# Kernel tuning notes

Measured on AMD Instinct MI355X. Metric: run time of the kernel, lower is better.

Reference implementation:

```python
import math
import jax, jax.numpy as jnp
import numpy as np

B, N, E, R = 1024, 200, 256, 256

def _layernorm(x, g, b, eps=1e-5):
    mu = x.mean(-1, keepdims=True)
    var = ((x - mu) ** 2).mean(-1, keepdims=True)
    return (x - mu) / jnp.sqrt(var + eps) * g + b

def setup_inputs() -> dict:
    key = jax.random.key(0)
    ks = jax.random.split(key, 16)
    d = {}
    d["e_emb"] = jax.random.normal(ks[0], (B, E), jnp.float32)
    d["nb_rel"] = jax.random.normal(ks[1], (B, N, R), jnp.float32)
    d["delta_t"] = jax.random.uniform(ks[2], (B, N), jnp.float32) * 10.0
    d["r_emb"] = jax.random.normal(ks[3], (B, R), jnp.float32)
    d["hist_mask"] = jax.random.randint(ks[4], (B, N), 0, 2).astype(bool)
    d["rel_w"] = jax.random.normal(ks[5], (E, R), jnp.float32) / math.sqrt(R)
    d["log_tau1"] = jnp.asarray(1.0, jnp.float32)
    d["log_tau2"] = jnp.asarray(2.5, jnp.float32)
    d["sharpness"] = jnp.asarray(1.5, jnp.float32)
    d["log_gamma"] = jnp.asarray(-2.0, jnp.float32)
    d["attn_w"] = jax.random.normal(ks[6], (3, E, E), jnp.float32) / math.sqrt(E)
    d["sp_w"] = jax.random.normal(ks[7], (3, E, 6 * E), jnp.float32) / math.sqrt(6 * E)
    d["sp_b"] = jnp.zeros((3, E), jnp.float32)
    d["ln_g"] = jnp.ones((3, E), jnp.float32)
    d["ln_b"] = jnp.zeros((3, E), jnp.float32)
    d["csq_w"] = jax.random.normal(ks[8], (E, R), jnp.float32) / math.sqrt(R)
    d["csq_b"] = jnp.zeros((E,), jnp.float32)
    d["csl_w"] = jax.random.normal(ks[9], (3, E), jnp.float32) / math.sqrt(E)
    d["csl_b"] = jnp.zeros((3,), jnp.float32)
    d["on_g"] = jnp.ones((E,), jnp.float32)
    d["on_b"] = jnp.zeros((E,), jnp.float32)
    return d

def _pna_one_scale(msgs, mask, e_emb, q_key, attn_w, sp_w, sp_b, ln_g, ln_b):
    # msgs: [B,N,E], mask: [B,N] bool, e_emb: [B,E], q_key: [B,E]
    valid_f = mask[..., None].astype(msgs.dtype)
    n_valid = jnp.maximum(mask.astype(msgs.dtype).sum(1, keepdims=True), 1.0)  # [B,1]
    msgs_v = msgs * valid_f
    mean_v = msgs_v.sum(1) / n_valid
    max_v = msgs_v.max(1)
    min_v = jnp.clip(jnp.where(mask[..., None], msgs, 10000.0).min(1), -10000.0, 10000.0)
    sq_m = (jnp.clip(msgs_v, -10.0, 10.0) ** 2).sum(1) / n_valid
    std_v = jnp.sqrt(jnp.maximum(sq_m - mean_v ** 2, 1e-6))
    q_proj = q_key @ attn_w.T  # [B,E]
    attn_raw = jnp.einsum('bne,be->bn', msgs, q_proj) / math.sqrt(msgs.shape[-1])
    attn_raw = jnp.where(mask, attn_raw, -10000.0)
    all_invalid = ~mask.any(1, keepdims=True)  # [B,1]
    attn_raw = jnp.where(all_invalid, 0.0, attn_raw)
    attn_p = jax.nn.softmax(attn_raw, axis=-1)
    attn_v = jnp.einsum('bn,bne->be', attn_p, msgs)
    feats = jnp.concatenate([mean_v, max_v, min_v, std_v, attn_v, e_emb], axis=-1)  # [B,6E]
    h = feats @ sp_w.T + sp_b
    h = _layernorm(h, ln_g, ln_b)
    return jax.nn.gelu(h, approximate=False)  # dropout = identity (eval mode)

def reference(e_emb, nb_rel, delta_t, r_emb, hist_mask, rel_w, log_tau1, log_tau2,
              sharpness, log_gamma, attn_w, sp_w, sp_b, ln_g, ln_b,
              csq_w, csq_b, csl_w, csl_b, on_g, on_b):
    msgs = jnp.einsum('bnr,er->bne', nb_rel, rel_w)
    gamma = jnp.exp(log_gamma)
    decay = jnp.exp(-gamma * jnp.maximum(delta_t, 0.0))
    msgs_dec = msgs * decay[..., None]
    tau1 = jnp.exp(log_tau1)
    tau2 = jnp.exp(log_tau2) + tau1
    sharp = jnp.clip(sharpness, 0.1, 5.0)
    w_fine = jax.nn.sigmoid(-sharp * (delta_t - tau1))
    w_coarse = jax.nn.sigmoid(sharp * (delta_t - tau2))
    w_mid = jnp.maximum(1.0 - w_fine - w_coarse, 0.0)
    scale_w = jnp.stack([w_fine, w_mid, w_coarse])  # [3,B,N]
    m_scales = msgs_dec[None] * scale_w[..., None]  # [3,B,N,E]
    q_key = r_emb @ rel_w.T  # [B,E]
    pna_v = jax.vmap(_pna_one_scale, in_axes=(0, None, None, None, 0, 0, 0, 0, 0))
    scales = pna_v(m_scales, hist_mask, e_emb, q_key, attn_w, sp_w, sp_b, ln_g, ln_b)  # [3,B,E]
    sq = r_emb @ csq_w.T + csq_b  # [B,E]
    logits = sq @ csl_w.T + csl_b  # [B,3]
    weights = jax.nn.softmax(logits, axis=-1)
    out = jnp.einsum('bs,sbe->be', weights, scales)
    return _layernorm(out, on_g, on_b)  # drop = identity (eval)
```

## Files before the change

### kernel.cpp

```cpp
#include <hip/hip_runtime.h>
#include <hip/hip_bf16.h>
#include <math.h>

#define B_   1024
#define N_   200
#define NR_  208
#define NT_  13
#define E_   256
#define R_   256
#define K6_  1536

typedef __attribute__((ext_vector_type(8))) short bf16x8;
typedef __attribute__((ext_vector_type(4))) float f32x4;

__device__ __forceinline__ unsigned short f2bf(float f) {
  unsigned int u = __float_as_uint(f);
  u += 0x7fffu + ((u >> 16) & 1u);
  return (unsigned short)(u >> 16);
}

__device__ __forceinline__ unsigned int pk_bf(float lo, float hi) {
  float2 t; t.x = lo; t.y = hi;
  __hip_bfloat162 h = __float22bfloat162_rn(t);
  unsigned int u;
  __builtin_memcpy(&u, &h, 4);
  return u;
}

__device__ __forceinline__ float gelu_exact(float x) {
  return 0.5f * x * (1.f + erff(x * 0.70710678118654752f));
}

__global__ __launch_bounds__(256) void k_cast(
    const float* __restrict__ rel_w, const float* __restrict__ sp_w,
    const float* __restrict__ csq_w, const float* __restrict__ attn_w,
    unsigned short* __restrict__ rwf, unsigned short* __restrict__ spwf,
    float* __restrict__ rwT, float* __restrict__ cwT, float* __restrict__ awT) {
  int o = blockIdx.x * 256 + threadIdx.x;
  if (o < 65536) {
    int j = o & 7, r16 = (o >> 3) & 15, quad = (o >> 7) & 3, ks = (o >> 9) & 7, et = o >> 12;
    rwf[o] = f2bf(rel_w[(size_t)(et * 16 + r16) * 256 + ks * 32 + quad * 8 + j]);
    return;
  }
  o -= 65536;
  if (o < 1179648) {
    int j = o & 7, r16 = (o >> 3) & 15, quad = (o >> 7) & 3, ks = (o >> 9) & 7;
    int rest = o >> 12;
    int kc = rest % 6, se = rest / 6;
    int et = se & 15, s = se >> 4;
    spwf[o] = f2bf(sp_w[(size_t)(s * 256 + et * 16 + r16) * 1536 + kc * 256 + ks * 32 + quad * 8 + j]);
    return;
  }
  o -= 1179648;
  if (o < 65536) { int r = o >> 8, e = o & 255; rwT[o] = rel_w[(size_t)e * 256 + r]; return; }
  o -= 65536;
  if (o < 65536) { int r = o >> 8, e = o & 255; cwT[o] = csq_w[(size_t)e * 256 + r]; return; }
  o -= 65536;
  if (o < 196608) {
    int s = o >> 16, rem = o & 65535, ep = rem >> 8, e = rem & 255;
    awT[o] = attn_w[((size_t)s * 256 + e) * 256 + ep];
  }
}

__global__ __launch_bounds__(256) void k_prep(
    const float* __restrict__ r_emb, const float* __restrict__ rwT,
    const float* __restrict__ cwT, const float* __restrict__ awT,
    const float* __restrict__ csq_b, const float* __restrict__ csl_w,
    const float* __restrict__ csl_b, const float* __restrict__ rel_w,
    unsigned short* __restrict__ t_bf, float* __restrict__ wts) {
  __shared__ __align__(16) float re[4][256];
  __shared__ __align__(16) float qk[4][256];
  __shared__ __align__(16) float sqs[4][256];
  __shared__ __align__(16) float qp[3][4][256];
  __shared__ float lg[4][3];
  int b0 = blockIdx.x * 4;
  int tid = threadIdx.x;
  int e = tid;
#pragma unroll
  for (int i = 0; i < 4; ++i)
    re[i][tid] = r_emb[(size_t)(b0 + i) * 256 + tid];
  __syncthreads();
  {
    float qkv[4], sv[4];
#pragma unroll
    for (int i = 0; i < 4; ++i) { qkv[i] = 0.f; sv[i] = 0.f; }
    for (int g = 0; g < 64; ++g) {
      float4 xi[4];
#pragma unroll
      for (int i = 0; i < 4; ++i) xi[i] = ((const float4*)re[i])[g];
#pragma unroll
      for (int k = 0; k < 4; ++k) {
        int r = g * 4 + k;
        float w = rwT[(size_t)r * 256 + e];
        float c = cwT[(size_t)r * 256 + e];
#pragma unroll
        for (int i = 0; i < 4; ++i) {
          float x = (k == 0) ? xi[i].x : (k == 1) ? xi[i].y : (k == 2) ? xi[i].z : xi[i].w;
          qkv[i] = fmaf(w, x, qkv[i]);
          sv[i]  = fmaf(c, x, sv[i]);
        }
      }
    }
    float cb = csq_b[e];
#pragma unroll
    for (int i = 0; i < 4; ++i) {
      qk[i][e] = qkv[i];
      sqs[i][e] = sv[i] + cb;
    }
  }
  __syncthreads();
  if (tid < 12) {
    int i = tid / 3, k = tid % 3;
    float acc = csl_b[k];
    for (int ee = 0; ee < 256; ++ee) acc += sqs[i][ee] * csl_w[k * 256 + ee];
    lg[i][k] = acc;
  }
  __syncthreads();
  if (tid < 4) {
    float l0 = lg[tid][0], l1 = lg[tid][1], l2 = lg[tid][2];
    float m = fmaxf(l0, fmaxf(l1, l2));
    float e0 = expf(l0 - m), e1 = expf(l1 - m), e2 = expf(l2 - m);
    float inv = 1.f / (e0 + e1 + e2);
    wts[(b0 + tid) * 4 + 0] = e0 * inv;
    wts[(b0 + tid) * 4 + 1] = e1 * inv;
    wts[(b0 + tid) * 4 + 2] = e2 * inv;
  }
  {
    float qpv[3][4];
#pragma unroll
    for (int s = 0; s < 3; ++s)
#pragma unroll
      for (int i = 0; i < 4; ++i) qpv[s][i] = 0.f;
    for (int g = 0; g < 64; ++g) {
      float4 qf[4];
#pragma unroll
      for (int i = 0; i < 4; ++i) qf[i] = ((const float4*)qk[i])[g];
#pragma unroll
      for (int k = 0; k < 4; ++k) {
        int ep = g * 4 + k;
#pragma unroll
        for (int s = 0; s < 3; ++s) {
          float w = awT[((size_t)s * 256 + ep) * 256 + e];
#pragma unroll
          for (int i = 0; i < 4; ++i) {
            float x = (k == 0) ? qf[i].x : (k == 1) ? qf[i].y : (k == 2) ? qf[i].z : qf[i].w;
            qpv[s][i] = fmaf(w, x, qpv[s][i]);
          }
        }
      }
    }
    __syncthreads();
#pragma unroll
    for (int s = 0; s < 3; ++s)
#pragma unroll
      for (int i = 0; i < 4; ++i) qp[s][i][e] = qpv[s][i];
  }
  __syncthreads();
  {
    int r = tid;
    float tacc[3][4];
#pragma unroll
    for (int s = 0; s < 3; ++s)
#pragma unroll
      for (int i = 0; i < 4; ++i) tacc[s][i] = 0.f;
    for (int e4 = 0; e4 < 64; ++e4) {
      float4 qv[3][4];
#pragma unroll
      for (int s = 0; s < 3; ++s)
#pragma unroll
        for (int i = 0; i < 4; ++i)
          qv[s][i] = ((const float4*)qp[s][i])[e4];
#pragma unroll
      for (int j = 0; j < 4; ++j) {
        float w = rel_w[(size_t)(e4 * 4 + j) * 256 + r];
#pragma unroll
        for (int s = 0; s < 3; ++s)
#pragma unroll
          for (int i = 0; i < 4; ++i) {
            float q = (j == 0) ? qv[s][i].x : (j == 1) ? qv[s][i].y
                      : (j == 2) ? qv[s][i].z : qv[s][i].w;
            tacc[s][i] = fmaf(q, w, tacc[s][i]);
          }
      }
    }
#pragma unroll
    for (int s = 0; s < 3; ++s)
#pragma unroll
      for (int i = 0; i < 4; ++i)
        t_bf[((size_t)(b0 + i) * 3 + s) * 256 + r] = f2bf(tacc[s][i]);
  }
}

__global__ __launch_bounds__(1024, 4) void k1_main(
    const float* __restrict__ nb_rel, const float* __restrict__ delta_t,
    const unsigned char* __restrict__ hm_raw, const float* __restrict__ e_emb,
    const float* __restrict__ p_lt1, const float* __restrict__ p_lt2,
    const float* __restrict__ p_sh, const float* __restrict__ p_lgm,
    const unsigned short* __restrict__ rwf, const unsigned short* __restrict__ t_bf,
    unsigned short* __restrict__ feats) {
  __shared__ __align__(16) struct {
    unsigned int a[NR_ * 132];
    float c[3][NR_];
    float p[3][NR_];
    float nmeta[NR_ * 12];
  } sm;
  int b = blockIdx.x;
  int tid = threadIdx.x;
  int lane = tid & 63, wave = tid >> 6;
  int row16 = lane & 15, quad = lane >> 4;

  int hasNZoff = 0, hasFP = 0;
  {
    unsigned char cc = hm_raw[tid];
    if ((tid & 3) != 0 && cc != 0) {
      hasNZoff = 1;
      if (cc == 0x3Fu || cc == 0x80u) hasFP = 1;
    }
  }
  int cntNZ = __syncthreads_count(hasNZoff);
  int cntFP = __syncthreads_count(hasFP);
  int mmode = (cntNZ == 0) ? 0 : (cntFP > 0 ? 2 : 1);

  float tau1 = __expf(p_lt1[0]);
  float tau2 = __expf(p_lt2[0]) + tau1;
  float sharp = fminf(fmaxf(p_sh[0], 0.1f), 5.0f);
  float gamma = __expf(p_lgm[0]);

  bool mk = false;
  if (tid < NR_) {
    float mf = 0.f, c0 = 0.f, c1 = 0.f, c2 = 0.f;
    if (tid < N_) {
      size_t mi = (size_t)b * N_ + tid;
      if (mmode == 0)      mk = ((const int*)hm_raw)[mi] != 0;
      else if (mmode == 1) mk = hm_raw[mi] != 0;
      else                 mk = ((const float*)hm_raw)[mi] != 0.f;
      float dt = delta_t[mi];
      mf = mk ? 1.f : 0.f;
      float decay = __expf(-gamma * fmaxf(dt, 0.f));
      float wf = 1.f / (1.f + __expf(sharp * (dt - tau1)));
      float wc = 1.f / (1.f + __expf(-sharp * (dt - tau2)));
      float wm = fmaxf(1.f - wf - wc, 0.f);
      c0 = decay * wf; c1 = decay * wm; c2 = decay * wc;
    }
    sm.c[0][tid] = c0; sm.c[1][tid] = c1; sm.c[2][tid] = c2;
    f32x4 w0, w1;
    w0[0] = mf * c0; w0[1] = mf * c1; w0[2] = mf * c2; w0[3] = mk ? 0.f : 1e4f;
    w1[0] = 0.f; w1[1] = 0.f; w1[2] = 0.f; w1[3] = mf;
    *(f32x4*)&sm.nmeta[tid * 12]     = w0;
    *(f32x4*)&sm.nmeta[tid * 12 + 4] = w1;
  }
  int cnt = __syncthreads_count(mk ? 1 : 0);
  float nvf = fmaxf((float)cnt, 1.f);
  bool allinv = (cnt == 0);

  {
    const float* src = nb_rel + (size_t)b * N_ * 256;
    float4 xs[NT_];
#pragma unroll
    for (int i = 0; i < NT_; ++i) {
      int n = i * 16 + wave;
      int gn = (n < N_) ? n : (N_ - 1);
      xs[i] = *(const float4*)(src + (size_t)gn * 256 + lane * 4);
    }
#pragma unroll
    for (int i = 0; i < NT_; ++i) {
      uint2 pk;
      pk.x = pk_bf(xs[i].x, xs[i].y);
      pk.y = pk_bf(xs[i].z, xs[i].w);
      *(uint2*)&sm.a[(i * 16 + wave) * 132 + lane * 2] = pk;
    }
  }
  __syncthreads();

  if (wave < NT_) {
    bf16x8 tfrag[8];
    {
      int sr = (row16 < 3) ? row16 : 0;
      const unsigned short* tb = t_bf + ((size_t)b * 3 + sr) * 256 + quad * 8;
      bf16x8 zer = {0, 0, 0, 0, 0, 0, 0, 0};
#pragma unroll
      for (int ks = 0; ks < 8; ++ks) {
        bf16x8 tv = *(const bf16x8*)(tb + ks * 32);
        tfrag[ks] = (row16 < 3) ? tv : zer;
      }
    }
    f32x4 acc;
#pragma unroll
    for (int cc = 0; cc < 4; ++cc) acc[cc] = 0.f;
#pragma unroll
    for (int ks = 0; ks < 8; ++ks) {
      bf16x8 af = *(const bf16x8*)&sm.a[(wave * 16 + row16) * 132 + ks * 16 + quad * 4];
      acc = __builtin_amdgcn_mfma_f32_16x16x32_bf16(af, tfrag[ks], acc, 0, 0, 0);
    }
    if (row16 < 3) {
#pragma unroll
      for (int rg = 0; rg < 4; ++rg) {
        int n = wave * 16 + quad * 4 + rg;
        float cw = sm.c[row16][n];
        float mf = sm.nmeta[n * 12 + 7];
        float l = cw * acc[rg] * 0.0625f;
        l = (mf > 0.5f) ? l : -1e4f;
        if (allinv) l = (n < N_) ? 0.f : -1e4f;
        sm.p[row16][n] = l;
      }
    }
  } else if (wave == NT_) {
    for (int i = lane; i < 256; i += 64) {
      unsigned short v = f2bf(e_emb[(size_t)b * 256 + i]);
      feats[((size_t)0 * B_ + b) * K6_ + 1280 + i] = v;
      feats[((size_t)1 * B_ + b) * K6_ + 1280 + i] = v;
      feats[((size_t)2 * B_ + b) * K6_ + 1280 + i] = v;
    }
  }

  bf16x8 bfr[8];
  {
#pragma unroll
    for (int ks = 0; ks < 8; ++ks)
      bfr[ks] = *(const bf16x8*)(rwf + ((((size_t)wave * 8 + ks) * 4 + quad) * 16 + row16) * 8);
  }
  __syncthreads();

  if (wave < 3) {
    int s = wave;
    float m = -1e30f;
    for (int n = lane; n < NR_; n += 64) m = fmaxf(m, sm.p[s][n]);
#pragma unroll
    for (int o = 32; o >= 1; o >>= 1) m = fmaxf(m, __shfl_xor(m, o, 64));
    float ssum = 0.f;
    for (int n = lane; n < NR_; n += 64) {
      float ev = __expf(sm.p[s][n] - m);
      sm.p[s][n] = ev;
      ssum += ev;
    }
#pragma unroll
    for (int o = 32; o >= 1; o >>= 1) ssum += __shfl_xor(ssum, o, 64);
    float inv = 1.f / ssum;
    for (int n = lane; n < NR_; n += 64)
      sm.nmeta[n * 12 + 4 + s] = sm.p[s][n] * inv * sm.c[s][n];
  }
  __syncthreads();

  float s_mean[3], s_mx[3], s_mn[3], s_sq[3], s_av[3];
#pragma unroll
  for (int s = 0; s < 3; ++s) {
    s_mean[s] = 0.f; s_mx[s] = -1e30f; s_mn[s] = 1e30f;
    s_sq[s] = 0.f; s_av[s] = 0.f;
  }

  for (int nt = 0; nt < NT_; ++nt) {
    f32x4 acc;
#pragma unroll
    for (int cc = 0; cc < 4; ++cc) acc[cc] = 0.f;
#pragma unroll
    for (int ks = 0; ks < 8; ++ks) {
      bf16x8 af = *(const bf16x8*)&sm.a[(nt * 16 + row16) * 132 + ks * 16 + quad * 4];
      acc = __builtin_amdgcn_mfma_f32_16x16x32_bf16(af, bfr[ks], acc, 0, 0, 0);
    }
    int nb = nt * 16 + quad * 4;
#pragma unroll
    for (int rg = 0; rg < 4; ++rg) {
      const float* nm = &sm.nmeta[(size_t)(nb + rg) * 12];
      f32x4 w0 = *(const f32x4*)nm;
      f32x4 w1 = *(const f32x4*)(nm + 4);
      float m = acc[rg];
#pragma unroll
      for (int s = 0; s < 3; ++s) {
        float vm = w0[s] * m;
        s_mean[s] += vm;
        s_mx[s] = fmaxf(s_mx[s], vm);
        s_mn[s] = fminf(s_mn[s], fmaf(w0[s], m, w0[3]));
        float cv = fminf(fmaxf(vm, -10.f), 10.f);
        s_sq[s] = fmaf(cv, cv, s_sq[s]);
        s_av[s] = fmaf(w1[s], m, s_av[s]);
      }
    }
  }

#pragma unroll
  for (int s = 0; s < 3; ++s) {
    float vmean = s_mean[s];
    vmean += __shfl_xor(vmean, 16, 64); vmean += __shfl_xor(vmean, 32, 64);
    float vmx = s_mx[s];
    vmx = fmaxf(vmx, __shfl_xor(vmx, 16, 64)); vmx = fmaxf(vmx, __shfl_xor(vmx, 32, 64));
    float vmn = s_mn[s];
    vmn = fminf(vmn, __shfl_xor(vmn, 16, 64)); vmn = fminf(vmn, __shfl_xor(vmn, 32, 64));
    float vsq = s_sq[s];
    vsq += __shfl_xor(vsq, 16, 64); vsq += __shfl_xor(vsq, 32, 64);
    float vav = s_av[s];
    vav += __shfl_xor(vav, 16, 64); vav += __shfl_xor(vav, 32, 64);
    if (lane < 16) {
      int e = wave * 16 + lane;
      size_t base = ((size_t)s * B_ + b) * K6_;
      float meanv = vmean / nvf;
      float stdv = sqrtf(fmaxf(vsq / nvf - meanv * meanv, 1e-6f));
      float mnv = fminf(fmaxf(vmn, -1e4f), 1e4f);
      feats[base + e] = f2bf(meanv);
      feats[base + 256 + e] = f2bf(vmx);
      feats[base + 512 + e] = f2bf(mnv);
      feats[base + 768 + e] = f2bf(stdv);
      feats[base + 1024 + e] = f2bf(vav);
    }
  }
}

__global__ __launch_bounds__(256) void k2_kernel(
    const unsigned short* __restrict__ feats, const unsigned short* __restrict__ spwf,
    const float* __restrict__ sp_b, float* __restrict__ hbuf) {
  __shared__ __align__(16) unsigned short A[16][1544];
  int id = blockIdx.x;
  int s = id >> 8;
  int rem = id & 255;
  int b0 = (rem >> 2) * 16;
  int e0 = (rem & 3) * 64;
  int tid = threadIdx.x, lane = tid & 63, wave = tid >> 6;
  int row16 = lane & 15, quad = lane >> 4;

  bf16x8 v[12];
#pragma unroll
  for (int t = 0; t < 12; ++t) {
    int j = tid + t * 256;
    int rw = j / 192, ck = j % 192;
    v[t] = *(const bf16x8*)(feats + ((size_t)s * B_ + b0 + rw) * K6_ + ck * 8);
  }
#pragma unroll
  for (int t = 0; t < 12; ++t) {
    int j = tid + t * 256;
    int rw = j / 192, ck = j % 192;
    *(bf16x8*)&A[rw][ck * 8] = v[t];
  }
  __syncthreads();

  int et = (e0 >> 4) + wave;
  const unsigned short* bp = spwf + (((size_t)s * 16 + et) * 6) * 4096;
  f32x4 acc;
#pragma unroll
  for (int cc = 0; cc < 4; ++cc) acc[cc] = 0.f;
#pragma unroll
  for (int kc = 0; kc < 6; ++kc) {
#pragma unroll
    for (int ks = 0; ks < 8; ++ks) {
      bf16x8 af = *(const bf16x8*)&A[row16][kc * 256 + ks * 32 + quad * 8];
      bf16x8 bf = *(const bf16x8*)(bp + ((size_t)(kc * 8 + ks) * 4 + quad) * 128 + row16 * 8);
      acc = __builtin_amdgcn_mfma_f32_16x16x32_bf16(af, bf, acc, 0, 0, 0);
    }
  }
  {
    int e = e0 + wave * 16 + row16;
    float bias = sp_b[s * 256 + e];
#pragma unroll
    for (int rg = 0; rg < 4; ++rg) {
      int rw = quad * 4 + rg;
      hbuf[((size_t)s * B_ + b0 + rw) * 256 + e] = acc[rg] + bias;
    }
  }
}

__global__ __launch_bounds__(256) void k3_kernel(
    const float* __restrict__ hbuf, const float* __restrict__ wts,
    const float* __restrict__ ln_g, const float* __restrict__ ln_b,
    const float* __restrict__ on_g, const float* __restrict__ on_b,
    float* __restrict__ out) {
  __shared__ float rs[4], rq[4];
  int b = blockIdx.x, tid = threadIdx.x, lane = tid & 63, wave = tid >> 6;
  float o = 0.f;
#pragma unroll
  for (int s = 0; s < 3; ++s) {
    float h = hbuf[((size_t)s * B_ + b) * 256 + tid];
    float sum = h, sq = h * h;
#pragma unroll
    for (int off = 32; off >= 1; off >>= 1) {
      sum += __shfl_xor(sum, off, 64);
      sq += __shfl_xor(sq, off, 64);
    }
    if (lane == 0) { rs[wave] = sum; rq[wave] = sq; }
    __syncthreads();
    float ts = rs[0] + rs[1] + rs[2] + rs[3];
    float tq = rq[0] + rq[1] + rq[2] + rq[3];
    __syncthreads();
    float mu = ts * (1.f / 256.f);
    float var = tq * (1.f / 256.f) - mu * mu;
    float rstd = rsqrtf(var + 1e-5f);
    float v = (h - mu) * rstd * ln_g[s * 256 + tid] + ln_b[s * 256 + tid];
    o += wts[b * 4 + s] * gelu_exact(v);
  }
  float sum = o, sq = o * o;
#pragma unroll
  for (int off = 32; off >= 1; off >>= 1) {
    sum += __shfl_xor(sum, off, 64);
    sq += __shfl_xor(sq, off, 64);
  }
  if (lane == 0) { rs[wave] = sum; rq[wave] = sq; }
  __syncthreads();
  float ts = rs[0] + rs[1] + rs[2] + rs[3];
  float tq = rq[0] + rq[1] + rq[2] + rq[3];
  float mu = ts * (1.f / 256.f);
  float var = tq * (1.f / 256.f) - mu * mu;
  float rstd = rsqrtf(var + 1e-5f);
  out[(size_t)b * 256 + tid] = (o - mu) * rstd * on_g[tid] + on_b[tid];
}

extern "C" void kernel_launch(void* const* d_in, const int* in_sizes, int n_in,
                              void* d_out, int out_size, void* d_ws, size_t ws_size,
                              hipStream_t stream) {
  const float* e_emb   = (const float*)d_in[0];
  const float* nb_rel  = (const float*)d_in[1];
  const float* delta_t = (const float*)d_in[2];
  const float* r_emb   = (const float*)d_in[3];
  const unsigned char* hist_mask = (const unsigned char*)d_in[4];
  const float* rel_w   = (const float*)d_in[5];
  const float* lt1     = (const float*)d_in[6];
  const float* lt2     = (const float*)d_in[7];
  const float* shp     = (const float*)d_in[8];
  const float* lgm     = (const float*)d_in[9];
  const float* attn_w  = (const float*)d_in[10];
  const float* sp_w    = (const float*)d_in[11];
  const float* sp_b    = (const float*)d_in[12];
  const float* ln_g    = (const float*)d_in[13];
  const float* ln_b    = (const float*)d_in[14];
  const float* csq_w   = (const float*)d_in[15];
  const float* csq_b   = (const float*)d_in[16];
  const float* csl_w   = (const float*)d_in[17];
  const float* csl_b   = (const float*)d_in[18];
  const float* on_g    = (const float*)d_in[19];
  const float* on_b    = (const float*)d_in[20];
  float* out = (float*)d_out;

  char* ws = (char*)d_ws;
  unsigned short* rwf   = (unsigned short*)(ws + 0);
  unsigned short* spwf  = (unsigned short*)(ws + 131072);
  unsigned short* t_bf  = (unsigned short*)(ws + 2490368);
  float* wts    = (float*)(ws + 4063232);
  unsigned short* feats = (unsigned short*)(ws + 4079616);
  float* hbuf   = (float*)(ws + 13516800);
  float* rwT    = (float*)(ws + 16662528);
  float* cwT    = (float*)(ws + 16924672);
  float* awT    = (float*)(ws + 17186816);

  hipLaunchKernelGGL(k_cast, dim3(6144), dim3(256), 0, stream, rel_w, sp_w, csq_w, attn_w,
                     rwf, spwf, rwT, cwT, awT);
  hipLaunchKernelGGL(k_prep, dim3(256), dim3(256), 0, stream, r_emb, rwT, cwT, awT,
                     csq_b, csl_w, csl_b, rel_w, t_bf, wts);
  hipLaunchKernelGGL(k1_main, dim3(1024), dim3(1024), 0, stream, nb_rel, delta_t, hist_mask,
                     e_emb, lt1, lt2, shp, lgm, rwf, t_bf, feats);
  hipLaunchKernelGGL(k2_kernel, dim3(768), dim3(256), 0, stream, feats, spwf, sp_b, hbuf);
  hipLaunchKernelGGL(k3_kernel, dim3(1024), dim3(256), 0, stream, hbuf, wts, ln_g, ln_b,
                     on_g, on_b, out);
}
```

Before: 484.2 us.

## Split prep kernel into three stages with two rows per block

The single prep kernel, which handled 4 batch rows per block in 256 blocks, becomes three kernels (q_key/sq plus softmax weights, attention projection, rel_w back-projection). Each handles 2 rows per block over 512 blocks, with intermediates staged in the feats and hbuf workspace buffers. The logits reduction now uses wave shuffles instead of 12 serial threads. The aim is more blocks across CUs and shorter dependent chains, at the cost of two extra launches, more global round trips, and weights reread by twice as many blocks.

```diff
diff --git a/kernel.cpp b/kernel.cpp
--- a/kernel.cpp
+++ b/kernel.cpp
@@ -62,133 +62,142 @@
   }
 }
 
-__global__ __launch_bounds__(256) void k_prep(
+__global__ __launch_bounds__(256) void k_prep1(
     const float* __restrict__ r_emb, const float* __restrict__ rwT,
-    const float* __restrict__ cwT, const float* __restrict__ awT,
-    const float* __restrict__ csq_b, const float* __restrict__ csl_w,
-    const float* __restrict__ csl_b, const float* __restrict__ rel_w,
-    unsigned short* __restrict__ t_bf, float* __restrict__ wts) {
-  __shared__ __align__(16) float re[4][256];
-  __shared__ __align__(16) float qk[4][256];
-  __shared__ __align__(16) float sqs[4][256];
-  __shared__ __align__(16) float qp[3][4][256];
-  __shared__ float lg[4][3];
-  int b0 = blockIdx.x * 4;
+    const float* __restrict__ cwT, const float* __restrict__ csq_b,
+    const float* __restrict__ csl_w, const float* __restrict__ csl_b,
+    float* __restrict__ qk_ws, float* __restrict__ wts) {
+  __shared__ __align__(16) float re[2][256];
+  __shared__ float sqs[2][256];
+  __shared__ float red[2][3][4];
+  int b0 = blockIdx.x * 2;
+  int tid = threadIdx.x, lane = tid & 63, wave = tid >> 6;
+  int e = tid;
+#pragma unroll
+  for (int i = 0; i < 2; ++i)
+    re[i][tid] = r_emb[(size_t)(b0 + i) * 256 + tid];
+  __syncthreads();
+  float qkv[2] = {0.f, 0.f}, sv[2] = {0.f, 0.f};
+  for (int g = 0; g < 64; ++g) {
+    float4 x0 = ((const float4*)re[0])[g];
+    float4 x1 = ((const float4*)re[1])[g];
+#pragma unroll
+    for (int k = 0; k < 4; ++k) {
+      int r = g * 4 + k;
+      float w = rwT[(size_t)r * 256 + e];
+      float c = cwT[(size_t)r * 256 + e];
+      float xa = (k == 0) ? x0.x : (k == 1) ? x0.y : (k == 2) ? x0.z : x0.w;
+      float xb = (k == 0) ? x1.x : (k == 1) ? x1.y : (k == 2) ? x1.z : x1.w;
+      qkv[0] = fmaf(w, xa, qkv[0]); qkv[1] = fmaf(w, xb, qkv[1]);
+      sv[0]  = fmaf(c, xa, sv[0]);  sv[1]  = fmaf(c, xb, sv[1]);
+    }
+  }
+  float cb = csq_b[e];
+#pragma unroll
+  for (int i = 0; i < 2; ++i) {
+    qk_ws[(size_t)(b0 + i) * 256 + e] = qkv[i];
+    sqs[i][e] = sv[i] + cb;
+  }
+  __syncthreads();
+#pragma unroll
+  for (int i = 0; i < 2; ++i)
+#pragma unroll
+    for (int k = 0; k < 3; ++k) {
+      float v = sqs[i][tid] * csl_w[k * 256 + tid];
+#pragma unroll
+      for (int o = 32; o >= 1; o >>= 1) v += __shfl_xor(v, o, 64);
+      if (lane == 0) red[i][k][wave] = v;
+    }
+  __syncthreads();
+  if (tid < 2) {
+    int i = tid;
+    float l[3];
+#pragma unroll
+    for (int k = 0; k < 3; ++k)
+      l[k] = csl_b[k] + red[i][k][0] + red[i][k][1] + red[i][k][2] + red[i][k][3];
+    float m = fmaxf(l[0], fmaxf(l[1], l[2]));
+    float e0 = expf(l[0] - m), e1 = expf(l[1] - m), e2 = expf(l[2] - m);
+    float inv = 1.f / (e0 + e1 + e2);
+    wts[(b0 + i) * 4 + 0] = e0 * inv;
+    wts[(b0 + i) * 4 + 1] = e1 * inv;
+    wts[(b0 + i) * 4 + 2] = e2 * inv;
+  }
+}
+
+__global__ __launch_bounds__(256) void k_prep2(
+    const float* __restrict__ qk_ws, const float* __restrict__ awT,
+    float* __restrict__ qp_ws) {
+  __shared__ __align__(16) float qk[2][256];
+  int b0 = blockIdx.x * 2;
   int tid = threadIdx.x;
   int e = tid;
 #pragma unroll
-  for (int i = 0; i < 4; ++i)
-    re[i][tid] = r_emb[(size_t)(b0 + i) * 256 + tid];
-  __syncthreads();
-  {
-    float qkv[4], sv[4];
-#pragma unroll
-    for (int i = 0; i < 4; ++i) { qkv[i] = 0.f; sv[i] = 0.f; }
-    for (int g = 0; g < 64; ++g) {
-      float4 xi[4];
-#pragma unroll
-      for (int i = 0; i < 4; ++i) xi[i] = ((const float4*)re[i])[g];
-#pragma unroll
-      for (int k = 0; k < 4; ++k) {
-        int r = g * 4 + k;
-        float w = rwT[(size_t)r * 256 + e];
-        float c = cwT[(size_t)r * 256 + e];
-#pragma unroll
-        for (int i = 0; i < 4; ++i) {
-          float x = (k == 0) ? xi[i].x : (k == 1) ? xi[i].y : (k == 2) ? xi[i].z : xi[i].w;
-          qkv[i] = fmaf(w, x, qkv[i]);
-          sv[i]  = fmaf(c, x, sv[i]);
-        }
+  for (int i = 0; i < 2; ++i)
+    qk[i][tid] = qk_ws[(size_t)(b0 + i) * 256 + tid];
+  __syncthreads();
+  float qpv[3][2];
+#pragma unroll
+  for (int s = 0; s < 3; ++s) { qpv[s][0] = 0.f; qpv[s][1] = 0.f; }
+  for (int g = 0; g < 64; ++g) {
+    float4 q0 = ((const float4*)qk[0])[g];
+    float4 q1 = ((const float4*)qk[1])[g];
+#pragma unroll
+    for (int k = 0; k < 4; ++k) {
+      int ep = g * 4 + k;
+      float xa = (k == 0) ? q0.x : (k == 1) ? q0.y : (k == 2) ? q0.z : q0.w;
+      float xb = (k == 0) ? q1.x : (k == 1) ? q1.y : (k == 2) ? q1.z : q1.w;
+#pragma unroll
+      for (int s = 0; s < 3; ++s) {
+        float w = awT[((size_t)s * 256 + ep) * 256 + e];
+        qpv[s][0] = fmaf(w, xa, qpv[s][0]);
+        qpv[s][1] = fmaf(w, xb, qpv[s][1]);
       }
     }
-    float cb = csq_b[e];
-#pragma unroll
-    for (int i = 0; i < 4; ++i) {
-      qk[i][e] = qkv[i];
-      sqs[i][e] = sv[i] + cb;
-    }
-  }
-  __syncthreads();
-  if (tid < 12) {
-    int i = tid / 3, k = tid % 3;
-    float acc = csl_b[k];
-    for (int ee = 0; ee < 256; ++ee) acc += sqs[i][ee] * csl_w[k * 256 + ee];
-    lg[i][k] = acc;
-  }
-  __syncthreads();
-  if (tid < 4) {
-    float l0 = lg[tid][0], l1 = lg[tid][1], l2 = lg[tid][2];
-    float m = fmaxf(l0, fmaxf(l1, l2));
-    float e0 = expf(l0 - m), e1 = expf(l1 - m), e2 = expf(l2 - m);
-    float inv = 1.f / (e0 + e1 + e2);
-    wts[(b0 + tid) * 4 + 0] = e0 * inv;
-    wts[(b0 + tid) * 4 + 1] = e1 * inv;
-    wts[(b0 + tid) * 4 + 2] = e2 * inv;
-  }
-  {
-    float qpv[3][4];
+  }
+#pragma unroll
+  for (int i = 0; i < 2; ++i)
 #pragma unroll
     for (int s = 0; s < 3; ++s)
-#pragma unroll
-      for (int i = 0; i < 4; ++i) qpv[s][i] = 0.f;
-    for (int g = 0; g < 64; ++g) {
-      float4 qf[4];
-#pragma unroll
-      for (int i = 0; i < 4; ++i) qf[i] = ((const float4*)qk[i])[g];
-#pragma unroll
-      for (int k = 0; k < 4; ++k) {
-        int ep = g * 4 + k;
-#pragma unroll
-        for (int s = 0; s < 3; ++s) {
-          float w = awT[((size_t)s * 256 + ep) * 256 + e];
-#pragma unroll
-          for (int i = 0; i < 4; ++i) {
-            float x = (k == 0) ? qf[i].x : (k == 1) ? qf[i].y : (k == 2) ? qf[i].z : qf[i].w;
-            qpv[s][i] = fmaf(w, x, qpv[s][i]);
-          }
-        }
+      qp_ws[((size_t)(b0 + i) * 3 + s) * 256 + e] = qpv[s][i];
+}
+
+__global__ __launch_bounds__(256) void k_prep3(
+    const float* __restrict__ qp_ws, const float* __restrict__ rel_w,
+    unsigned short* __restrict__ t_bf) {
+  __shared__ __align__(16) float qp[2][3][256];
+  int b0 = blockIdx.x * 2;
+  int tid = threadIdx.x;
+  int r = tid;
+  for (int j = tid; j < 2 * 3 * 256; j += 256)
+    ((float*)qp)[j] = qp_ws[(size_t)b0 * 768 + j];
+  __syncthreads();
+  float tacc[3][2];
+#pragma unroll
+  for (int s = 0; s < 3; ++s) { tacc[s][0] = 0.f; tacc[s][1] = 0.f; }
+  for (int e4 = 0; e4 < 64; ++e4) {
+    float4 qv[3][2];
+#pragma unroll
+    for (int s = 0; s < 3; ++s) {
+      qv[s][0] = ((const float4*)qp[0][s])[e4];
+      qv[s][1] = ((const float4*)qp[1][s])[e4];
+    }
+#pragma unroll
+    for (int j = 0; j < 4; ++j) {
+      float w = rel_w[(size_t)(e4 * 4 + j) * 256 + r];
+#pragma unroll
+      for (int s = 0; s < 3; ++s) {
+        float qa = (j == 0) ? qv[s][0].x : (j == 1) ? qv[s][0].y : (j == 2) ? qv[s][0].z : qv[s][0].w;
+        float qb = (j == 0) ? qv[s][1].x : (j == 1) ? qv[s][1].y : (j == 2) ? qv[s][1].z : qv[s][1].w;
+        tacc[s][0] = fmaf(qa, w, tacc[s][0]);
+        tacc[s][1] = fmaf(qb, w, tacc[s][1]);
       }
     }
-    __syncthreads();
+  }
+#pragma unroll
+  for (int i = 0; i < 2; ++i)
 #pragma unroll
     for (int s = 0; s < 3; ++s)
-#pragma unroll
-      for (int i = 0; i < 4; ++i) qp[s][i][e] = qpv[s][i];
-  }
-  __syncthreads();
-  {
-    int r = tid;
-    float tacc[3][4];
-#pragma unroll
-    for (int s = 0; s < 3; ++s)
-#pragma unroll
-      for (int i = 0; i < 4; ++i) tacc[s][i] = 0.f;
-    for (int e4 = 0; e4 < 64; ++e4) {
-      float4 qv[3][4];
-#pragma unroll
-      for (int s = 0; s < 3; ++s)
-#pragma unroll
-        for (int i = 0; i < 4; ++i)
-          qv[s][i] = ((const float4*)qp[s][i])[e4];
-#pragma unroll
-      for (int j = 0; j < 4; ++j) {
-        float w = rel_w[(size_t)(e4 * 4 + j) * 256 + r];
-#pragma unroll
-        for (int s = 0; s < 3; ++s)
-#pragma unroll
-          for (int i = 0; i < 4; ++i) {
-            float q = (j == 0) ? qv[s][i].x : (j == 1) ? qv[s][i].y
-                      : (j == 2) ? qv[s][i].z : qv[s][i].w;
-            tacc[s][i] = fmaf(q, w, tacc[s][i]);
-          }
-      }
-    }
-#pragma unroll
-    for (int s = 0; s < 3; ++s)
-#pragma unroll
-      for (int i = 0; i < 4; ++i)
-        t_bf[((size_t)(b0 + i) * 3 + s) * 256 + r] = f2bf(tacc[s][i]);
-  }
+      t_bf[((size_t)(b0 + i) * 3 + s) * 256 + r] = f2bf(tacc[s][i]);
 }
 
 __global__ __launch_bounds__(1024, 4) void k1_main(
@@ -537,10 +546,15 @@
   float* cwT    = (float*)(ws + 16924672);
   float* awT    = (float*)(ws + 17186816);
 
+  float* qk_ws = (float*)feats;
+  float* qp_ws = hbuf;
+
   hipLaunchKernelGGL(k_cast, dim3(6144), dim3(256), 0, stream, rel_w, sp_w, csq_w, attn_w,
                      rwf, spwf, rwT, cwT, awT);
-  hipLaunchKernelGGL(k_prep, dim3(256), dim3(256), 0, stream, r_emb, rwT, cwT, awT,
-                     csq_b, csl_w, csl_b, rel_w, t_bf, wts);
+  hipLaunchKernelGGL(k_prep1, dim3(512), dim3(256), 0, stream, r_emb, rwT, cwT,
+                     csq_b, csl_w, csl_b, qk_ws, wts);
+  hipLaunchKernelGGL(k_prep2, dim3(512), dim3(256), 0, stream, qk_ws, awT, qp_ws);
+  hipLaunchKernelGGL(k_prep3, dim3(512), dim3(256), 0, stream, qp_ws, rel_w, t_bf);
   hipLaunchKernelGGL(k1_main, dim3(1024), dim3(1024), 0, stream, nb_rel, delta_t, hist_mask,
                      e_emb, lt1, lt2, shp, lgm, rwf, t_bf, feats);
   hipLaunchKernelGGL(k2_kernel, dim3(768), dim3(256), 0, stream, feats, spwf, sp_b, hbuf);
```

Result: faster. 474.0 us (-2.1%).
